# Optimization experiments

Measured on AMD Instinct MI355X. Metric: run time of the kernel, lower is better.

Reference implementation:

```python
import jax, jax.numpy as jnp
import numpy as np
from jax import lax

B, C, OUT, H, W = 8, 512, 512, 64, 64
BN_EPS = 1e-5


def setup_inputs() -> dict:
    key = jax.random.key(0)
    ks = jax.random.split(key, 20)
    s = 1.0 / np.sqrt(C)
    d = {
        "input1": jax.random.normal(ks[0], (B, C, H, W), jnp.float32),
        "input2": jax.random.normal(ks[1], (B, C, H, W), jnp.float32),
        "wq1": jax.random.normal(ks[2], (C, C), jnp.float32) * s,
        "bq1": jnp.zeros((C,), jnp.float32),
        "wk1": jax.random.normal(ks[3], (C, C), jnp.float32) * s,
        "bk1": jnp.zeros((C,), jnp.float32),
        "wv1": jax.random.normal(ks[4], (C, C), jnp.float32) * s,
        "bv1": jnp.zeros((C,), jnp.float32),
        "wq2": jax.random.normal(ks[5], (C, C), jnp.float32) * s,
        "bq2": jnp.zeros((C,), jnp.float32),
        "wk2": jax.random.normal(ks[6], (C, C), jnp.float32) * s,
        "bk2": jnp.zeros((C,), jnp.float32),
        "wv2": jax.random.normal(ks[7], (C, C), jnp.float32) * s,
        "bv2": jnp.zeros((C,), jnp.float32),
        "w_lin": jax.random.normal(ks[8], (1, C), jnp.float32) * s,  # shared gate conv, no bias
        "w_cat": jax.random.normal(ks[9], (OUT, 2 * C, 3, 3), jnp.float32) * (1.0 / np.sqrt(2 * C * 9)),
        "bn_gamma": jnp.ones((OUT,), jnp.float32),
        "bn_beta": jnp.zeros((OUT,), jnp.float32),
    }
    return d


def _conv1x1(x, w, b):
    # x: [B,C,H,W], w: [O,C] -> [B,O,H,W]
    return jnp.einsum('bchw,oc->bohw', x, w) + b[None, :, None, None]


def _branch(x_q_src, x_kv_src, wq, bq, wk, bk, wv, bv, w_lin, x_resid):
    # matches: attn = softmax(k(x_kv) @ q(x_q)^T); out = attn^T @ v(x_kv)
    b, c, h, w = x_kv_src.shape
    n = h * w
    q = _conv1x1(x_q_src, wq, bq).reshape(b, c, n)      # [B,C,N] (from the OTHER input)
    k = _conv1x1(x_kv_src, wk, bk).reshape(b, c, n)
    v = _conv1x1(x_kv_src, wv, bv).reshape(b, c, n)
    attn = jnp.einsum('bkn,bcn->bkc', k, q)             # [B,C,C]
    attn = jax.nn.softmax(attn, axis=-1)
    out = jnp.einsum('bkc,bkn->bcn', attn, v).reshape(b, c, h, w)
    # sigmoid gate: linear(avgpool(x_resid)) -> scalar per batch
    pooled = jnp.mean(x_resid, axis=(2, 3))             # [B,C]
    a = jax.nn.sigmoid(pooled @ w_lin.T)                # [B,1]
    return out * a[:, :, None, None] + x_resid


def reference(input1, input2, wq1, bq1, wk1, bk1, wv1, bv1,
              wq2, bq2, wk2, bk2, wv2, bv2, w_lin, w_cat, bn_gamma, bn_beta):
    # branch 1: k1 from input1, q2 from input2, v1 from input1, gate from input1
    out1 = _branch(input2, input1, wq2, bq2, wk1, bk1, wv1, bv1, w_lin, input1)
    # branch 2: k2 from input2, q1 from input1, v2 from input2, gate from input2
    out2 = _branch(input1, input2, wq1, bq1, wk2, bk2, wv2, bv2, w_lin, input2)
    x = jnp.concatenate([out1, out2], axis=1)           # [B,2C,H,W]
    y = lax.conv_general_dilated(x, w_cat, (1, 1), 'SAME',
                                 dimension_numbers=('NCHW', 'OIHW', 'NCHW'))
    # BatchNorm2d in training mode: batch statistics over (N,H,W)
    mean = jnp.mean(y, axis=(0, 2, 3), keepdims=True)
    var = jnp.var(y, axis=(0, 2, 3), keepdims=True)
    y = (y - mean) * lax.rsqrt(var + BN_EPS)
    y = y * bn_gamma[None, :, None, None] + bn_beta[None, :, None, None]
    return jax.nn.relu(y)
```

## Files before the change

### kernel.cpp

```cpp
#include <hip/hip_runtime.h>


typedef unsigned short u16;
typedef unsigned int u32;
typedef float f32x4 __attribute__((ext_vector_type(4)));
typedef short bf16x8 __attribute__((ext_vector_type(8)));

#define DEV __device__ __forceinline__

DEV u16 f2bf(float f) {
  u32 u = __float_as_uint(f);
  return (u16)((u + 0x7fffu + ((u >> 16) & 1u)) >> 16);
}
DEV float bf2f(u16 u) { return __uint_as_float(((u32)u) << 16); }

DEV void gload_lds16(const void* g, void* l) {
  __builtin_amdgcn_global_load_lds(
      (const __attribute__((address_space(1))) void*)g,
      (__attribute__((address_space(3))) void*)l, 16, 0, 0);
}

DEV void stage_tile(u16* L, const u16* src, int row0, long ld, int k0, int wid, int lane) {
  int rr = lane >> 2;
  int cc = (lane & 3) << 3;
#pragma unroll
  for (int j = 0; j < 2; ++j) {
    int chunk = j * 4 + wid;
    const u16* g = src + (long)(row0 + chunk * 16 + rr) * ld + (k0 + cc);
    gload_lds16(g, L + chunk * 512);
  }
}

DEV float waveRedSum(float v) {
#pragma unroll
  for (int o = 32; o > 0; o >>= 1) v += __shfl_xor(v, o);
  return v;
}

__global__ __launch_bounds__(256) void gemm_gramK(const float* __restrict__ X1,
                                                  const float* __restrict__ X2,
                                                  float* __restrict__ parts)
{
  __shared__ __align__(16) u16 lds[4 * 4096];
  const int bid = blockIdx.x;
  const int cid = ((bid & 7) << 6) + (bid >> 3);
  const int z = cid >> 4, xy = cid & 15;
  const int quarter = z >> 3, b = z & 7;
  const int m0 = (xy & 3) * 128, n0 = (xy >> 2) * 128;
  const int tid = threadIdx.x, wid = tid >> 6, lane = tid & 63;
  const int wr = wid >> 1, wc = wid & 1;
  const int r16 = lane & 15, koff = (lane >> 4) << 3;
  const float* A = X1 + (long)b * 2097152 + quarter * 1024;
  const float* Bp = X2 + (long)b * 2097152 + quarter * 1024;
  const int sr = tid >> 3;
  const int sc = (tid & 7) * 4;

  f32x4 acc[4][4];
#pragma unroll
  for (int i = 0; i < 4; ++i)
#pragma unroll
    for (int j = 0; j < 4; ++j) acc[i][j] = (f32x4){0.f, 0.f, 0.f, 0.f};

  for (int k0 = 0; k0 < 1024; k0 += 32) {
    __syncthreads();
#pragma unroll
    for (int rr = 0; rr < 128; rr += 32) {
      float4 va = *(const float4*)&A[(long)(m0 + rr + sr) * 4096 + k0 + sc];
      float4 vb = *(const float4*)&Bp[(long)(n0 + rr + sr) * 4096 + k0 + sc];
      float fa[4] = {va.x, va.y, va.z, va.w};
      float fb[4] = {vb.x, vb.y, vb.z, vb.w};
      u32 pah0 = 0, pah1 = 0, pal0 = 0, pal1 = 0;
      u32 pbh0 = 0, pbh1 = 0, pbl0 = 0, pbl1 = 0;
#pragma unroll
      for (int e = 0; e < 2; ++e) {
        u16 h = f2bf(fa[e]);      pah0 |= ((u32)h) << (16 * e);
        u16 lo = f2bf(fa[e] - bf2f(h)); pal0 |= ((u32)lo) << (16 * e);
        h = f2bf(fa[e + 2]);      pah1 |= ((u32)h) << (16 * e);
        lo = f2bf(fa[e + 2] - bf2f(h)); pal1 |= ((u32)lo) << (16 * e);
        h = f2bf(fb[e]);          pbh0 |= ((u32)h) << (16 * e);
        lo = f2bf(fb[e] - bf2f(h)); pbl0 |= ((u32)lo) << (16 * e);
        h = f2bf(fb[e + 2]);      pbh1 |= ((u32)h) << (16 * e);
        lo = f2bf(fb[e + 2] - bf2f(h)); pbl1 |= ((u32)lo) << (16 * e);
      }
      int off = (rr + sr) * 32 + sc;
      *(uint2*)&lds[off]         = make_uint2(pah0, pah1);
      *(uint2*)&lds[4096 + off]  = make_uint2(pal0, pal1);
      *(uint2*)&lds[8192 + off]  = make_uint2(pbh0, pbh1);
      *(uint2*)&lds[12288 + off] = make_uint2(pbl0, pbl1);
    }
    __syncthreads();
    bf16x8 ah[4], al[4], bh[4], bl[4];
#pragma unroll
    for (int mi = 0; mi < 4; ++mi) {
      ah[mi] = *(const bf16x8*)&lds[(wr * 64 + mi * 16 + r16) * 32 + koff];
      al[mi] = *(const bf16x8*)&lds[4096 + (wr * 64 + mi * 16 + r16) * 32 + koff];
    }
#pragma unroll
    for (int nj = 0; nj < 4; ++nj) {
      bh[nj] = *(const bf16x8*)&lds[8192 + (wc * 64 + nj * 16 + r16) * 32 + koff];
      bl[nj] = *(const bf16x8*)&lds[12288 + (wc * 64 + nj * 16 + r16) * 32 + koff];
    }
#pragma unroll
    for (int mi = 0; mi < 4; ++mi)
#pragma unroll
      for (int nj = 0; nj < 4; ++nj) {
        acc[mi][nj] = __builtin_amdgcn_mfma_f32_16x16x32_bf16(ah[mi], bh[nj], acc[mi][nj], 0, 0, 0);
        acc[mi][nj] = __builtin_amdgcn_mfma_f32_16x16x32_bf16(ah[mi], bl[nj], acc[mi][nj], 0, 0, 0);
        acc[mi][nj] = __builtin_amdgcn_mfma_f32_16x16x32_bf16(al[mi], bh[nj], acc[mi][nj], 0, 0, 0);
      }
  }

  const int rq = lane >> 4;
  float* O = parts + (long)z * 262144;
#pragma unroll
  for (int mi = 0; mi < 4; ++mi)
#pragma unroll
    for (int nj = 0; nj < 4; ++nj)
#pragma unroll
      for (int i = 0; i < 4; ++i) {
        int row = m0 + wr * 64 + mi * 16 + rq * 4 + i;
        int col = n0 + wc * 64 + nj * 16 + r16;
        O[(long)row * 512 + col] = acc[mi][nj][i];
      }
}

__global__ __launch_bounds__(256) void k_gsplit(const float* __restrict__ parts,
                                                u16* __restrict__ Gh, u16* __restrict__ Gl)
{
  for (long i = (long)blockIdx.x * 256 + threadIdx.x; i < 2097152; i += (long)gridDim.x * 256) {
    float v = parts[i] + parts[i + 2097152] + parts[i + 4194304] + parts[i + 6291456];
    u16 h = f2bf(v);
    Gh[i] = h;
    Gl[i] = f2bf(v - bf2f(h));
  }
}

constexpr int EP_SPLIT = 0, EP_LOGITS = 1, EP_BF16 = 2, EP_XCAT = 3;

struct GArgs {
  const u16* Ah[2]; const u16* Al[2];
  const u16* Bh[2]; const u16* Bl[2];
  long Az[2], Bz[2];
  void* O0[2]; void* O1[2];
  const float* f0[2]; const float* f1[2];
  const float* f2[2]; const float* f3[2];
  const u16* rptr[2];
};

template <int EP, bool SPLIT3, bool FLAT>
__global__ __launch_bounds__(256) void gemm_tn2(GArgs ga, int lda, int ldb, int K, long Oz)
{
  __shared__ __align__(16) u16 lds[(SPLIT3 ? 4 : 2) * 4096];
  int bx, by, z;
  if constexpr (FLAT) {
    const int cid = ((blockIdx.x & 7) << 8) + (blockIdx.x >> 3);
    z = cid >> 7;
    const int xy = cid & 127;
    bx = xy >> 2; by = xy & 3;
  } else {
    bx = blockIdx.x; by = blockIdx.y; z = blockIdx.z;
  }
  const int br = z >> 3, b = z & 7;
  const u16* pAh = ga.Ah[br] + (long)b * ga.Az[br];
  const u16* pBh = ga.Bh[br] + (long)b * ga.Bz[br];
  const u16* pAl = SPLIT3 ? ga.Al[br] + (long)b * ga.Az[br] : nullptr;
  const u16* pBl = SPLIT3 ? ga.Bl[br] + (long)b * ga.Bz[br] : nullptr;
  const int m0 = bx * 128, n0 = by * 128;
  const int tid = threadIdx.x, wid = tid >> 6, lane = tid & 63;
  const int wr = wid >> 1, wc = wid & 1;
  const int r16 = lane & 15, koff = (lane >> 4) << 3;

  f32x4 acc[4][4];
#pragma unroll
  for (int i = 0; i < 4; ++i)
#pragma unroll
    for (int j = 0; j < 4; ++j) acc[i][j] = (f32x4){0.f, 0.f, 0.f, 0.f};

  for (int k0 = 0; k0 < K; k0 += 32) {
    __syncthreads();
    stage_tile(lds, pAh, m0, lda, k0, wid, lane);
    stage_tile(lds + 4096, pBh, n0, ldb, k0, wid, lane);
    if constexpr (SPLIT3) {
      stage_tile(lds + 8192, pAl, m0, lda, k0, wid, lane);
      stage_tile(lds + 12288, pBl, n0, ldb, k0, wid, lane);
    }
    __syncthreads();
    bf16x8 af[4], bfh[4], af2[4], bf2_[4];
#pragma unroll
    for (int mi = 0; mi < 4; ++mi)
      af[mi] = *(const bf16x8*)&lds[(wr * 64 + mi * 16 + r16) * 32 + koff];
#pragma unroll
    for (int nj = 0; nj < 4; ++nj)
      bfh[nj] = *(const bf16x8*)&lds[4096 + (wc * 64 + nj * 16 + r16) * 32 + koff];
    if constexpr (SPLIT3) {
#pragma unroll
      for (int mi = 0; mi < 4; ++mi)
        af2[mi] = *(const bf16x8*)&lds[8192 + (wr * 64 + mi * 16 + r16) * 32 + koff];
#pragma unroll
      for (int nj = 0; nj < 4; ++nj)
        bf2_[nj] = *(const bf16x8*)&lds[12288 + (wc * 64 + nj * 16 + r16) * 32 + koff];
    }
#pragma unroll
    for (int mi = 0; mi < 4; ++mi)
#pragma unroll
      for (int nj = 0; nj < 4; ++nj) {
        acc[mi][nj] = __builtin_amdgcn_mfma_f32_16x16x32_bf16(af[mi], bfh[nj], acc[mi][nj], 0, 0, 0);
        if constexpr (SPLIT3) {
          acc[mi][nj] = __builtin_amdgcn_mfma_f32_16x16x32_bf16(af[mi], bf2_[nj], acc[mi][nj], 0, 0, 0);
          acc[mi][nj] = __builtin_amdgcn_mfma_f32_16x16x32_bf16(af2[mi], bfh[nj], acc[mi][nj], 0, 0, 0);
        }
      }
  }

  const int rq = lane >> 4;
  const long off = (long)z * Oz;
  float g = 0.f;
  if constexpr (EP == EP_XCAT) g = ga.f1[br][b];
#pragma unroll
  for (int mi = 0; mi < 4; ++mi)
#pragma unroll
    for (int nj = 0; nj < 4; ++nj)
#pragma unroll
      for (int i = 0; i < 4; ++i) {
        int row = m0 + wr * 64 + mi * 16 + rq * 4 + i;
        int col = n0 + wc * 64 + nj * 16 + r16;
        float v = acc[mi][nj][i];
        if constexpr (EP == EP_SPLIT) {
          long idx = off + (long)row * 512 + col;
          u16 h = f2bf(v);
          ((u16*)ga.O0[br])[idx] = h;
          ((u16*)ga.O1[br])[idx] = f2bf(v - bf2f(h));
        } else if constexpr (EP == EP_LOGITS) {
          v += ga.f0[br][row] * ga.f3[br][b * 512 + col] + ga.f1[br][col] * ga.f2[br][b * 512 + row];
          ((float*)ga.O0[br])[off + (long)row * 512 + col] = v;
        } else if constexpr (EP == EP_BF16) {
          ((u16*)ga.O0[br])[off + (long)row * 512 + col] = f2bf(v);
        } else {
          float val = (v + ga.f0[br][b * 512 + col]) * g +
                      bf2f(ga.rptr[br][(long)b * 2097152 + (long)row * 512 + col]);
          int yy = row >> 6, xx = row & 63;
          long oidx = ((long)(b * 66 + yy + 1) * 66 + (xx + 1)) * 512 + col;
          ((u16*)ga.O0[br])[oidx] = f2bf(val);
        }
      }
}

#define MF(a, b, c) __builtin_amdgcn_mfma_f32_16x16x32_bf16(a, b, c, 0, 0, 0)
#define SCHEDB() __builtin_amdgcn_sched_barrier(0)
#define BAR() __builtin_amdgcn_s_barrier()
#define STG_B(QB, i) gload_lds16(xb + sbo[i] + kko, &lds[(QB) + ldsB0 + (i) * 4096])
#define STG_A(QB, i) gload_lds16(Arow + (i) * 294912L + Aoff, &lds[(QB) + ldsA0 + (i) * 2048])

#define RD_A(d, fmb)                                                        \
  d##0 = *(const bf16x8*)&lds[pBase + aRd + (fmb) * 1024 + sxa0];           \
  d##1 = *(const bf16x8*)&lds[pBase + aRd + (fmb) * 1024 + sxa1];           \
  d##2 = *(const bf16x8*)&lds[pBase + aRd + ((fmb) + 1) * 1024 + sxa0];     \
  d##3 = *(const bf16x8*)&lds[pBase + aRd + ((fmb) + 1) * 1024 + sxa1];

#define MM(jj, r)                                                           \
  __builtin_amdgcn_s_setprio(1);                                            \
  _Pragma("unroll")                                                         \
  for (int fn = 0; fn < 4; ++fn) {                                          \
    acc[2 * (jj)][fn] = MF(r##0, bq[fn][0], acc[2 * (jj)][fn]);             \
    acc[2 * (jj)][fn] = MF(r##1, bq[fn][1], acc[2 * (jj)][fn]);             \
    acc[2 * (jj) + 1][fn] = MF(r##2, bq[fn][0], acc[2 * (jj) + 1][fn]);     \
    acc[2 * (jj) + 1][fn] = MF(r##3, bq[fn][1], acc[2 * (jj) + 1][fn]);     \
  }                                                                         \
  __builtin_amdgcn_s_setprio(0);                                            \
  SCHEDB();

__global__ __launch_bounds__(512, 2) void k_conv8(const u16* __restrict__ W,
                                                  const u16* __restrict__ xA,
                                                  const u16* __restrict__ xB,
                                                  float* __restrict__ y,
                                                  float* __restrict__ bnsum,
                                                  float* __restrict__ bnsum2)
{
  __shared__ __align__(16) u16 lds[65536];
  const int cid = ((blockIdx.x & 7) << 5) + (blockIdx.x >> 3);
  const int bz = cid >> 5, mx = (cid >> 4) & 1, ny = cid & 15;
  const int m0 = mx * 256, n0 = ny * 256;
  const long zoff = (long)bz * 2230272;

  const int tid = threadIdx.x;
  const int w = tid >> 6, l = tid & 63;
  const int wr = w >> 2, wcn = w & 3, wl = w & 3;
  const int lr = l >> 3, l7 = l & 7, l15 = l & 15, l4 = l >> 4;
  const int ss8 = (l7 ^ lr) << 3;

  long sbo[4];
#pragma unroll
  for (int i = 0; i < 4; ++i) {
    int n = n0 + i * 64 + w * 8 + lr;
    sbo[i] = (long)((n >> 6) * 66 + (n & 63)) * 512;
  }
  const u16* Arow = W + (long)(m0 + wr * 128 + wl * 8 + lr) * 9216 + ss8;
  const int ldsA0 = wr * 8192 + wl * 512;
  const int ldsB0 = 16384 + w * 512;
  const int sxa0 = (l4 ^ l7) << 3;
  const int sxa1 = ((l4 | 4) ^ l7) << 3;
  const int aRd = wr * 8192 + l15 * 64;
  const int bRd = 16384 + wcn * 4096 + l15 * 64;

  f32x4 acc[8][4];
#pragma unroll
  for (int i = 0; i < 8; ++i)
#pragma unroll
    for (int j = 0; j < 4; ++j) acc[i][j] = (f32x4){0.f, 0.f, 0.f, 0.f};

  {
    const u16* xb = xA + zoff;
    const long kko = ss8;
    const long Aoff = 0;
    STG_B(0, 0); STG_B(0, 1); STG_B(0, 2); STG_B(0, 3);
    STG_A(0, 0); STG_A(0, 1); STG_A(0, 2); STG_A(0, 3);
  }

  for (int t = 0; t < 144; ++t) {
    const int pBase = (t & 1) << 15;
    const int qBase = pBase ^ 32768;
    const int tau = t + 1;
    const bool pf = tau < 144;
    const int ccc = tau / 9;
    const int tap = tau - ccc * 9;
    const int cch = ccc << 6;
    const u16* xb = ((cch & 512) ? xB : xA) + zoff;
    const long kko = (long)((tap / 3) * 66 + (tap % 3)) * 512 + (cch & 511) + ss8;
    const long Aoff = (long)(tap << 10) + cch;
    bf16x8 bq[4][2];
    bf16x8 cA0, cA1, cA2, cA3, nA0, nA1, nA2, nA3;

    if (pf) { STG_B(qBase, 0); STG_B(qBase, 1); asm volatile("s_waitcnt vmcnt(4)" ::: "memory"); }
    else    { asm volatile("s_waitcnt vmcnt(2)" ::: "memory"); }
    BAR(); SCHEDB();
#pragma unroll
    for (int fn = 0; fn < 4; ++fn) {
      bq[fn][0] = *(const bf16x8*)&lds[pBase + bRd + fn * 1024 + sxa0];
      bq[fn][1] = *(const bf16x8*)&lds[pBase + bRd + fn * 1024 + sxa1];
    }
    RD_A(cA, 0)
    RD_A(nA, 2)
    MM(0, cA)
    if (pf) { STG_B(qBase, 2); STG_B(qBase, 3); asm volatile("s_waitcnt vmcnt(5)" ::: "memory"); }
    else    { asm volatile("s_waitcnt vmcnt(1)" ::: "memory"); }
    BAR(); SCHEDB();
    RD_A(cA, 4)
    MM(1, nA)
    if (pf) { STG_A(qBase, 0); STG_A(qBase, 1); asm volatile("s_waitcnt vmcnt(6)" ::: "memory"); }
    else    { asm volatile("s_waitcnt vmcnt(0)" ::: "memory"); }
    BAR(); SCHEDB();
    RD_A(nA, 6)
    MM(2, cA)
    if (pf) { STG_A(qBase, 2); STG_A(qBase, 3); }
    BAR(); SCHEDB();
    MM(3, nA)
  }

#pragma unroll
  for (int fm = 0; fm < 8; ++fm)
#pragma unroll
    for (int fn = 0; fn < 4; ++fn)
#pragma unroll
      for (int i = 0; i < 4; ++i) {
        int row = m0 + wr * 128 + fm * 16 + l4 * 4 + i;
        int col = n0 + wcn * 64 + fn * 16 + l15;
        y[((long)bz * 512 + row) * 4096 + col] = acc[fm][fn][i];
      }

  __syncthreads();
  float* fl = (float*)lds;
#pragma unroll
  for (int fm = 0; fm < 8; ++fm)
#pragma unroll
    for (int i = 0; i < 4; ++i) {
      float s = acc[fm][0][i] + acc[fm][1][i] + acc[fm][2][i] + acc[fm][3][i];
      float s2 = acc[fm][0][i] * acc[fm][0][i] + acc[fm][1][i] * acc[fm][1][i] +
                 acc[fm][2][i] * acc[fm][2][i] + acc[fm][3][i] * acc[fm][3][i];
#pragma unroll
      for (int m = 1; m < 16; m <<= 1) { s += __shfl_xor(s, m); s2 += __shfl_xor(s2, m); }
      if (l15 == 0) {
        int r = wr * 128 + fm * 16 + l4 * 4 + i;
        fl[r * 4 + wcn] = s;
        fl[1024 + r * 4 + wcn] = s2;
      }
    }
  __syncthreads();
  {
    int r = tid & 255;
    int which = tid >> 8;
    const float* p = fl + which * 1024 + r * 4;
    float v = p[0] + p[1] + p[2] + p[3];
    atomicAdd((which ? bnsum2 : bnsum) + m0 + r, v);
  }
}

struct PrepArgs {
  const float* wv1; const float* wv2;
  u16* WvT1; u16* WvT2;
  const float* s[4]; u16* h[4]; u16* l[4];
  const float* wcat; u16* wcp;
  u16* xcat;
  float* rsum; float* bnsum; float* mbz;
};

__global__ __launch_bounds__(256) void k_mprep(PrepArgs a)
{
  __shared__ __align__(16) float shbuf[9261];
  const int bx = blockIdx.x;
  const int tid = threadIdx.x;
  if (bx < 128) {
    const float* src = (bx < 64) ? a.wv1 : a.wv2;
    u16* dst = (bx < 64) ? a.WvT1 : a.WvT2;
    const int t8 = bx & 63;
    const int c0 = (t8 & 7) * 64, r0 = (t8 >> 3) * 64;
#pragma unroll
    for (int it = 0; it < 4; ++it) {
      int rr = it * 16 + (tid >> 4);
      int cc = (tid & 15) * 4;
      float4 v = *(const float4*)&src[(long)(r0 + rr) * 512 + c0 + cc];
      shbuf[rr * 65 + cc] = v.x; shbuf[rr * 65 + cc + 1] = v.y;
      shbuf[rr * 65 + cc + 2] = v.z; shbuf[rr * 65 + cc + 3] = v.w;
    }
    __syncthreads();
    int nr = tid >> 2, cs = (tid & 3) * 16;
    u16 hh[16] __attribute__((aligned(16)));
#pragma unroll
    for (int j = 0; j < 16; ++j) hh[j] = f2bf(shbuf[(cs + j) * 65 + nr]);
    long d = (long)(c0 + nr) * 512 + r0 + cs;
    *(uint4*)&dst[d] = *(const uint4*)&hh[0];
    *(uint4*)&dst[d + 8] = *(const uint4*)&hh[8];
  } else if (bx < 1152) {
    int which = (bx - 128) >> 8;
    const float* s = a.s[which];
    u16* h = a.h[which];
    u16* l = a.l[which];
    for (int i = ((bx - 128) & 255) * 256 + tid; i < 262144; i += 65536) {
      float v = s[i];
      u16 hh = f2bf(v);
      h[i] = hh;
      l[i] = f2bf(v - bf2f(hh));
    }
  } else if (bx < 1664) {
    const int o = bx - 1152;
    const float* s = a.wcat + (long)o * 9216;
#pragma unroll
    for (int it = 0; it < 9; ++it) {
      int f4 = it * 256 + tid;
      float4 v = *(const float4*)&s[f4 * 4];
      float va[4] = {v.x, v.y, v.z, v.w};
      int f = f4 * 4;
#pragma unroll
      for (int e = 0; e < 4; ++e) {
        int ic = (f + e) / 9, tp = (f + e) - ic * 9;
        shbuf[tp * 1029 + ic] = va[e];
      }
    }
    __syncthreads();
    u16* d = a.wcp + (long)o * 9216;
#pragma unroll
    for (int tp = 0; tp < 9; ++tp)
#pragma unroll
      for (int c = 0; c < 4; ++c) {
        int ic = c * 256 + tid;
        d[tp * 1024 + ic] = f2bf(shbuf[tp * 1029 + ic]);
      }
  } else if (bx < 1680) {
    const long base = (long)(bx - 1664) * 2230272;
    const uint4 z4 = make_uint4(0, 0, 0, 0);
    for (int i = tid; i < 8448; i += 256) {
      long off = (i < 4224) ? (long)i * 8 : (long)65 * 66 * 512 + (long)(i - 4224) * 8;
      *(uint4*)&a.xcat[base + off] = z4;
    }
    for (int i = tid; i < 8192; i += 256) {
      int y = 1 + (i >> 7);
      int xsel = (i >> 6) & 1;
      int v = i & 63;
      long off = ((long)y * 66 + (xsel ? 65 : 0)) * 512 + (long)v * 8;
      *(uint4*)&a.xcat[base + off] = z4;
    }
  } else {
    float4 f4 = {0.f, 0.f, 0.f, 0.f};
    for (int i = tid; i < 2048; i += 256) ((float4*)a.rsum)[i] = f4;
    for (int i = tid; i < 256; i += 256) ((float4*)a.bnsum)[i] = f4;
    for (int i = tid; i < 2048; i += 256) ((float4*)a.mbz)[i] = f4;
  }
}

__global__ __launch_bounds__(256) void k_prep(const float* __restrict__ in1,
                                              const float* __restrict__ in2,
                                              u16* __restrict__ xT1, u16* __restrict__ xT2,
                                              float* __restrict__ rsum)
{
  __shared__ float t[64][65];
  const int zz = blockIdx.z;
  const int inp = zz >> 3, b = zz & 7;
  const int cb = blockIdx.y, nb = blockIdx.x;
  const float* s = (inp ? in2 : in1) + (long)b * 2097152;
  u16* xT = inp ? xT2 : xT1;
  float* rs = rsum + inp * 4096;
  const int tid = threadIdx.x;
#pragma unroll
  for (int it = 0; it < 4; ++it) {
    int cr = it * 16 + (tid >> 4);
    int nc = (tid & 15) * 4;
    float4 v = *(const float4*)&s[(long)(cb * 64 + cr) * 4096 + nb * 64 + nc];
    t[cr][nc] = v.x; t[cr][nc + 1] = v.y; t[cr][nc + 2] = v.z; t[cr][nc + 3] = v.w;
  }
  __syncthreads();
  int nr = tid >> 2, cs = (tid & 3) * 16;
  u16 hh[16] __attribute__((aligned(16)));
#pragma unroll
  for (int j = 0; j < 16; ++j) hh[j] = f2bf(t[cs + j][nr]);
  long d = (long)b * 2097152 + (long)(nb * 64 + nr) * 512 + cb * 64 + cs;
  *(uint4*)&xT[d] = *(const uint4*)&hh[0];
  *(uint4*)&xT[d + 8] = *(const uint4*)&hh[8];
  if (tid < 64) {
    float sum = 0.f;
#pragma unroll 8
    for (int j = 0; j < 64; ++j) sum += t[tid][j];
    atomicAdd(&rs[b * 512 + tid + cb * 64], sum);
  }
}

__global__ __launch_bounds__(256) void k_skq(const float* __restrict__ wk1, const float* __restrict__ wq2,
                                             const float* __restrict__ wk2, const float* __restrict__ wq1,
                                             const float* __restrict__ bq2, const float* __restrict__ bq1,
                                             const float* __restrict__ wlin,
                                             const float* __restrict__ rowsum,
                                             float* __restrict__ S, float* __restrict__ gates)
{
  int which = blockIdx.y, b = blockIdx.z;
  int lane = threadIdx.x & 63;
  if (which == 4) {
    if (blockIdx.x < 2 && threadIdx.x < 64) {
      int inp = blockIdx.x;
      float s = 0.f;
      for (int c = lane; c < 512; c += 64) s += rowsum[inp * 4096 + b * 512 + c] * wlin[c];
      s = waveRedSum(s);
      if (lane == 0) gates[inp * 8 + b] = 1.f / (1.f + __expf(-s / 4096.f));
    }
    return;
  }
  int row = blockIdx.x * 4 + (threadIdx.x >> 6);
  const float* W; const float* rs; const float* bias = nullptr;
  if (which == 0)      { W = wk1; rs = rowsum + b * 512; }
  else if (which == 1) { W = wq2; rs = rowsum + 4096 + b * 512; bias = bq2; }
  else if (which == 2) { W = wk2; rs = rowsum + 4096 + b * 512; }
  else                 { W = wq1; rs = rowsum + b * 512; bias = bq1; }
  float s = 0.f;
  for (int i = lane; i < 512; i += 64) s += W[row * 512 + i] * rs[i];
  s = waveRedSum(s);
  if (lane == 0) S[(which * 8 + b) * 512 + row] = s + (bias ? 4096.f * bias[row] : 0.f);
}

__global__ __launch_bounds__(256) void k_softmaxT(const float* __restrict__ L,
                                                  u16* __restrict__ attnT,
                                                  const float* __restrict__ bv1,
                                                  const float* __restrict__ bv2,
                                                  float* __restrict__ mb)
{
  const int bid = blockIdx.x;
  const int z = bid >> 4, rg = bid & 15;
  const int w = threadIdx.x >> 6, lane = threadIdx.x & 63;
  const int a0 = rg * 32 + w * 8;
  const float* Lz = L + (long)z * 262144;
  const float* bv = (z >= 8) ? bv2 : bv1;
  u16* Az = attnT + (long)z * 262144;
  u32 pk[8][4] = {};
  float pmb[8] = {};
#pragma unroll
  for (int it = 0; it < 8; ++it) {
    long base = (long)(a0 + it) * 512 + lane * 8;
    float4 p0 = *(const float4*)&Lz[base], p1 = *(const float4*)&Lz[base + 4];
    float v[8] = {p0.x, p0.y, p0.z, p0.w, p1.x, p1.y, p1.z, p1.w};
    float m = v[0];
#pragma unroll
    for (int j = 1; j < 8; ++j) m = fmaxf(m, v[j]);
#pragma unroll
    for (int o = 32; o > 0; o >>= 1) m = fmaxf(m, __shfl_xor(m, o));
    float e[8], s = 0.f;
#pragma unroll
    for (int j = 0; j < 8; ++j) { e[j] = __expf(v[j] - m); s += e[j]; }
    s = waveRedSum(s);
    float inv = 1.f / s;
    float bvv = bv[a0 + it];
#pragma unroll
    for (int j = 0; j < 8; ++j) {
      float p = e[j] * inv;
      pk[j][it >> 1] |= ((u32)f2bf(p)) << ((it & 1) * 16);
      pmb[j] += p * bvv;
    }
  }
#pragma unroll
  for (int j = 0; j < 8; ++j) {
    int c = lane * 8 + j;
    *(uint4*)&Az[(long)c * 512 + a0] = make_uint4(pk[j][0], pk[j][1], pk[j][2], pk[j][3]);
    atomicAdd(&mb[z * 512 + c], pmb[j]);
  }
}

__global__ __launch_bounds__(256) void k_bnapply(float* __restrict__ y,
                                                 const float* __restrict__ bnsum,
                                                 const float* __restrict__ bnsum2,
                                                 const float* __restrict__ gamma,
                                                 const float* __restrict__ beta)
{
  const long n = 16777216;
  for (long i = ((long)blockIdx.x * 256 + threadIdx.x) * 4; i < n; i += (long)gridDim.x * 1024) {
    float4 v = *(const float4*)&y[i];
    int o = (int)((i >> 12) & 511);
    float mean = bnsum[o] * (1.f / 32768.f);
    float var = bnsum2[o] * (1.f / 32768.f) - mean * mean;
    float a = gamma[o] * rsqrtf(var + 1e-5f);
    float c = beta[o] - mean * a;
    v.x = fmaxf(v.x * a + c, 0.f);
    v.y = fmaxf(v.y * a + c, 0.f);
    v.z = fmaxf(v.z * a + c, 0.f);
    v.w = fmaxf(v.w * a + c, 0.f);
    *(float4*)&y[i] = v;
  }
}

extern "C" void kernel_launch(void* const* d_in, const int* in_sizes, int n_in,
                              void* d_out, int out_size, void* d_ws, size_t ws_size,
                              hipStream_t stream)
{
  (void)in_sizes; (void)n_in; (void)out_size; (void)ws_size;
  const float* in1 = (const float*)d_in[0];
  const float* in2 = (const float*)d_in[1];
  const float* wq1 = (const float*)d_in[2];  const float* bq1 = (const float*)d_in[3];
  const float* wk1 = (const float*)d_in[4];  const float* bk1 = (const float*)d_in[5];
  const float* wv1 = (const float*)d_in[6];  const float* bv1 = (const float*)d_in[7];
  const float* wq2 = (const float*)d_in[8];  const float* bq2 = (const float*)d_in[9];
  const float* wk2 = (const float*)d_in[10]; const float* bk2 = (const float*)d_in[11];
  const float* wv2 = (const float*)d_in[12]; const float* bv2 = (const float*)d_in[13];
  const float* wlin  = (const float*)d_in[14];
  const float* wcat  = (const float*)d_in[15];
  const float* gamma = (const float*)d_in[16];
  const float* beta  = (const float*)d_in[17];

  char* ws = (char*)d_ws;
  const size_t MB = 1024ull * 1024ull;
  u16* Gh     = (u16*)(ws + 0 * MB);
  u16* Gl     = (u16*)(ws + 4 * MB);
  u16* Mb     = (u16*)(ws + 0 * MB);
  u16* Uh     = (u16*)(ws + 8 * MB);
  u16* attnT  = (u16*)(ws + 8 * MB);
  u16* Ul     = (u16*)(ws + 16 * MB);
  float* logits = (float*)(ws + 24 * MB);
  float* parts  = (float*)(ws + 8 * MB);
  u16* xcatA  = (u16*)(ws + 40 * MB);
  u16* xcatB  = xcatA + 8L * 2230272;
  u16* wcp    = (u16*)(ws + 112 * MB);
  u16* wsp    = (u16*)(ws + 122 * MB);
  u16* WvT1   = (u16*)(ws + 126 * MB);
  u16* WvT2   = WvT1 + 262144;
  float* rowsum = (float*)(ws + 127 * MB);
  float* gates  = (float*)(ws + 127 * MB + 32 * 1024);
  float* S      = (float*)(ws + 127 * MB + 36 * 1024);
  float* mb     = (float*)(ws + 127 * MB + 100 * 1024);
  float* bnsum  = (float*)(ws + 127 * MB + 132 * 1024);
  float* bnsum2 = (float*)(ws + 127 * MB + 134 * 1024);

  u16* wq1h = wsp + 0 * 262144; u16* wq1l = wsp + 1 * 262144;
  u16* wq2h = wsp + 2 * 262144; u16* wq2l = wsp + 3 * 262144;
  u16* wk1h = wsp + 4 * 262144; u16* wk1l = wsp + 5 * 262144;
  u16* wk2h = wsp + 6 * 262144; u16* wk2l = wsp + 7 * 262144;

  u16* xT1 = (u16*)d_out;
  u16* xT2 = (u16*)d_out + 16777216;
  float* ybuf = (float*)d_out;

  {
    PrepArgs pa;
    pa.wv1 = wv1; pa.wv2 = wv2; pa.WvT1 = WvT1; pa.WvT2 = WvT2;
    pa.s[0] = wq1; pa.h[0] = wq1h; pa.l[0] = wq1l;
    pa.s[1] = wq2; pa.h[1] = wq2h; pa.l[1] = wq2l;
    pa.s[2] = wk1; pa.h[2] = wk1h; pa.l[2] = wk1l;
    pa.s[3] = wk2; pa.h[3] = wk2h; pa.l[3] = wk2l;
    pa.wcat = wcat; pa.wcp = wcp;
    pa.xcat = xcatA;
    pa.rsum = rowsum; pa.bnsum = bnsum; pa.mbz = mb;
    k_mprep<<<1681, 256, 0, stream>>>(pa);
  }
  k_prep<<<dim3(64, 8, 16), 256, 0, stream>>>(in1, in2, xT1, xT2, rowsum);
  k_skq<<<dim3(128, 5, 8), 256, 0, stream>>>(wk1, wq2, wk2, wq1, bq2, bq1, wlin, rowsum, S, gates);

  gemm_gramK<<<512, 256, 0, stream>>>(in1, in2, parts);
  k_gsplit<<<2048, 256, 0, stream>>>(parts, Gh, Gl);

  {
    GArgs ga = {};
    ga.Ah[0] = wq2h; ga.Al[0] = wq2l; ga.Ah[1] = wk2h; ga.Al[1] = wk2l;
    ga.Az[0] = 0; ga.Az[1] = 0;
    ga.Bh[0] = Gh; ga.Bl[0] = Gl; ga.Bh[1] = Gh; ga.Bl[1] = Gl;
    ga.Bz[0] = 262144; ga.Bz[1] = 262144;
    ga.O0[0] = Uh; ga.O0[1] = Uh; ga.O1[0] = Ul; ga.O1[1] = Ul;
    gemm_tn2<EP_SPLIT, true, false><<<dim3(4, 4, 16), 256, 0, stream>>>(ga, 512, 512, 512, 262144);
  }
  {
    GArgs ga = {};
    ga.Ah[0] = wk1h; ga.Al[0] = wk1l; ga.Az[0] = 0;
    ga.Ah[1] = Uh + 2097152; ga.Al[1] = Ul + 2097152; ga.Az[1] = 262144;
    ga.Bh[0] = Uh; ga.Bl[0] = Ul; ga.Bz[0] = 262144;
    ga.Bh[1] = wq1h; ga.Bl[1] = wq1l; ga.Bz[1] = 0;
    ga.O0[0] = logits; ga.O0[1] = logits;
    ga.f0[0] = bk1; ga.f1[0] = bq2; ga.f2[0] = S;        ga.f3[0] = S + 4096;
    ga.f0[1] = bk2; ga.f1[1] = bq1; ga.f2[1] = S + 8192; ga.f3[1] = S + 12288;
    gemm_tn2<EP_LOGITS, true, false><<<dim3(4, 4, 16), 256, 0, stream>>>(ga, 512, 512, 512, 262144);
  }
  k_softmaxT<<<256, 256, 0, stream>>>(logits, attnT, bv1, bv2, mb);
  {
    GArgs ga = {};
    ga.Ah[0] = attnT; ga.Ah[1] = attnT + 2097152;
    ga.Az[0] = 262144; ga.Az[1] = 262144;
    ga.Bh[0] = WvT1; ga.Bh[1] = WvT2; ga.Bz[0] = 0; ga.Bz[1] = 0;
    ga.O0[0] = Mb; ga.O0[1] = Mb;
    gemm_tn2<EP_BF16, false, false><<<dim3(4, 4, 16), 256, 0, stream>>>(ga, 512, 512, 512, 262144);
  }
  {
    GArgs ga = {};
    ga.Ah[0] = xT1; ga.Ah[1] = xT2; ga.Az[0] = 2097152; ga.Az[1] = 2097152;
    ga.Bh[0] = Mb; ga.Bh[1] = Mb + 2097152; ga.Bz[0] = 262144; ga.Bz[1] = 262144;
    ga.O0[0] = xcatA; ga.O0[1] = xcatB;
    ga.f0[0] = mb; ga.f0[1] = mb + 4096;
    ga.f1[0] = gates; ga.f1[1] = gates + 8;
    ga.rptr[0] = xT1; ga.rptr[1] = xT2;
    gemm_tn2<EP_XCAT, false, true><<<2048, 256, 0, stream>>>(ga, 512, 512, 512, 0);
  }

  k_conv8<<<256, 512, 0, stream>>>(wcp, xcatA, xcatB, ybuf, bnsum, bnsum2);
  k_bnapply<<<4096, 256, 0, stream>>>(ybuf, bnsum, bnsum2, gamma, beta);
}
```

Before: 601.2 us.

## Fuse BatchNorm apply into conv via grid barrier and swizzle GEMM LDS tiles

The conv kernel now keeps its accumulators in registers, waits at a global atomic-counter barrier until all 256 blocks have added their BN partial sums, then applies the BN scale/shift and ReLU before a single store. This removes the separate bnapply pass that re-read and re-wrote the 64 MB output. The zeroing loop is widened to also clear the counter. Separately, the GEMM LDS tiles get an XOR swizzle on the k-chunk index to reduce bank conflicts on fragment reads. The grid barrier assumes all 256 blocks are co-resident, which 256 CUs at 2 blocks per CU should allow. Blocks also sit idle while waiting for the slowest one.

Result: slower. 643.2 us (+7.0%).

```diff
diff --git a/kernel.cpp b/kernel.cpp
--- a/kernel.cpp
+++ b/kernel.cpp
@@ -22,7 +22,7 @@
 
 DEV void stage_tile(u16* L, const u16* src, int row0, long ld, int k0, int wid, int lane) {
   int rr = lane >> 2;
-  int cc = (lane & 3) << 3;
+  int cc = (((lane & 3) ^ (rr & 3)) << 3);
 #pragma unroll
   for (int j = 0; j < 2; ++j) {
     int chunk = j * 4 + wid;
@@ -49,11 +49,14 @@
   const int m0 = (xy & 3) * 128, n0 = (xy >> 2) * 128;
   const int tid = threadIdx.x, wid = tid >> 6, lane = tid & 63;
   const int wr = wid >> 1, wc = wid & 1;
-  const int r16 = lane & 15, koff = (lane >> 4) << 3;
+  const int r16 = lane & 15;
+  const int koff = (((lane >> 4) ^ (r16 & 3)) << 3);
   const float* A = X1 + (long)b * 2097152 + quarter * 1024;
   const float* Bp = X2 + (long)b * 2097152 + quarter * 1024;
   const int sr = tid >> 3;
   const int sc = (tid & 7) * 4;
+  const int s8 = (tid & 7) >> 1, hf = tid & 1;
+  const int swoff = ((s8 ^ (sr & 3)) << 3) + hf * 4;
 
   f32x4 acc[4][4];
 #pragma unroll
@@ -82,7 +85,7 @@
         h = f2bf(fb[e + 2]);      pbh1 |= ((u32)h) << (16 * e);
         lo = f2bf(fb[e + 2] - bf2f(h)); pbl1 |= ((u32)lo) << (16 * e);
       }
-      int off = (rr + sr) * 32 + sc;
+      int off = (rr + sr) * 32 + swoff;
       *(uint2*)&lds[off]         = make_uint2(pah0, pah1);
       *(uint2*)&lds[4096 + off]  = make_uint2(pal0, pal1);
       *(uint2*)&lds[8192 + off]  = make_uint2(pbh0, pbh1);
@@ -168,7 +171,8 @@
   const int m0 = bx * 128, n0 = by * 128;
   const int tid = threadIdx.x, wid = tid >> 6, lane = tid & 63;
   const int wr = wid >> 1, wc = wid & 1;
-  const int r16 = lane & 15, koff = (lane >> 4) << 3;
+  const int r16 = lane & 15;
+  const int koff = (((lane >> 4) ^ (r16 & 3)) << 3);
 
   f32x4 acc[4][4];
 #pragma unroll
@@ -274,7 +278,10 @@
                                                   const u16* __restrict__ xB,
                                                   float* __restrict__ y,
                                                   float* __restrict__ bnsum,
-                                                  float* __restrict__ bnsum2)
+                                                  float* __restrict__ bnsum2,
+                                                  const float* __restrict__ gamma,
+                                                  const float* __restrict__ beta,
+                                                  int* __restrict__ cnt)
 {
   __shared__ __align__(16) u16 lds[65536];
   const int cid = ((blockIdx.x & 7) << 5) + (blockIdx.x >> 3);
@@ -356,17 +363,6 @@
     MM(3, nA)
   }
 
-#pragma unroll
-  for (int fm = 0; fm < 8; ++fm)
-#pragma unroll
-    for (int fn = 0; fn < 4; ++fn)
-#pragma unroll
-      for (int i = 0; i < 4; ++i) {
-        int row = m0 + wr * 128 + fm * 16 + l4 * 4 + i;
-        int col = n0 + wcn * 64 + fn * 16 + l15;
-        y[((long)bz * 512 + row) * 4096 + col] = acc[fm][fn][i];
-      }
-
   __syncthreads();
   float* fl = (float*)lds;
 #pragma unroll
@@ -392,6 +388,37 @@
     float v = p[0] + p[1] + p[2] + p[3];
     atomicAdd((which ? bnsum2 : bnsum) + m0 + r, v);
   }
+  __threadfence();
+  __syncthreads();
+  if (tid == 0) {
+    atomicAdd(cnt, 1);
+    while (atomicAdd(cnt, 0) < 256) __builtin_amdgcn_s_sleep(16);
+  }
+  __syncthreads();
+  __threadfence();
+  if (tid < 256) {
+    int ch = m0 + tid;
+    float s1 = atomicAdd(&bnsum[ch], 0.f);
+    float s2 = atomicAdd(&bnsum2[ch], 0.f);
+    float mean = s1 * (1.f / 32768.f);
+    float var = s2 * (1.f / 32768.f) - mean * mean;
+    float a = gamma[ch] * rsqrtf(var + 1e-5f);
+    fl[2048 + tid] = a;
+    fl[2304 + tid] = beta[ch] - mean * a;
+  }
+  __syncthreads();
+#pragma unroll
+  for (int fm = 0; fm < 8; ++fm)
+#pragma unroll
+    for (int i = 0; i < 4; ++i) {
+      int rl = wr * 128 + fm * 16 + l4 * 4 + i;
+      float a = fl[2048 + rl], c = fl[2304 + rl];
+#pragma unroll
+      for (int fn = 0; fn < 4; ++fn) {
+        int col = n0 + wcn * 64 + fn * 16 + l15;
+        y[((long)bz * 512 + m0 + rl) * 4096 + col] = fmaxf(acc[fm][fn][i] * a + c, 0.f);
+      }
+    }
 }
 
 struct PrepArgs {
@@ -481,7 +508,7 @@
   } else {
     float4 f4 = {0.f, 0.f, 0.f, 0.f};
     for (int i = tid; i < 2048; i += 256) ((float4*)a.rsum)[i] = f4;
-    for (int i = tid; i < 256; i += 256) ((float4*)a.bnsum)[i] = f4;
+    for (int i = tid; i < 257; i += 256) ((float4*)a.bnsum)[i] = f4;
     for (int i = tid; i < 2048; i += 256) ((float4*)a.mbz)[i] = f4;
   }
 }
@@ -596,28 +623,6 @@
     int c = lane * 8 + j;
     *(uint4*)&Az[(long)c * 512 + a0] = make_uint4(pk[j][0], pk[j][1], pk[j][2], pk[j][3]);
     atomicAdd(&mb[z * 512 + c], pmb[j]);
-  }
-}
-
-__global__ __launch_bounds__(256) void k_bnapply(float* __restrict__ y,
-                                                 const float* __restrict__ bnsum,
-                                                 const float* __restrict__ bnsum2,
-                                                 const float* __restrict__ gamma,
-                                                 const float* __restrict__ beta)
-{
-  const long n = 16777216;
-  for (long i = ((long)blockIdx.x * 256 + threadIdx.x) * 4; i < n; i += (long)gridDim.x * 1024) {
-    float4 v = *(const float4*)&y[i];
-    int o = (int)((i >> 12) & 511);
-    float mean = bnsum[o] * (1.f / 32768.f);
-    float var = bnsum2[o] * (1.f / 32768.f) - mean * mean;
-    float a = gamma[o] * rsqrtf(var + 1e-5f);
-    float c = beta[o] - mean * a;
-    v.x = fmaxf(v.x * a + c, 0.f);
-    v.y = fmaxf(v.y * a + c, 0.f);
-    v.z = fmaxf(v.z * a + c, 0.f);
-    v.w = fmaxf(v.w * a + c, 0.f);
-    *(float4*)&y[i] = v;
   }
 }
 
@@ -661,6 +666,7 @@
   float* mb     = (float*)(ws + 127 * MB + 100 * 1024);
   float* bnsum  = (float*)(ws + 127 * MB + 132 * 1024);
   float* bnsum2 = (float*)(ws + 127 * MB + 134 * 1024);
+  int*   cnt    = (int*)(ws + 127 * MB + 136 * 1024);
 
   u16* wq1h = wsp + 0 * 262144; u16* wq1l = wsp + 1 * 262144;
   u16* wq2h = wsp + 2 * 262144; u16* wq2l = wsp + 3 * 262144;
@@ -729,6 +735,5 @@
     gemm_tn2<EP_XCAT, false, true><<<2048, 256, 0, stream>>>(ga, 512, 512, 512, 0);
   }
 
-  k_conv8<<<256, 512, 0, stream>>>(wcp, xcatA, xcatB, ybuf, bnsum, bnsum2);
-  k_bnapply<<<4096, 256, 0, stream>>>(ybuf, bnsum, bnsum2, gamma, beta);
-}
+  k_conv8<<<256, 512, 0, stream>>>(wcp, xcatA, xcatB, ybuf, bnsum, bnsum2, gamma, beta, cnt);
+}
```
